# Kernel optimization log

Hardware: AMD Instinct MI355X
Metric: run time of the kernel (lower is better)

Reference implementation:

```python
import jax, jax.numpy as jnp
import numpy as np

N, E, B = 8000, 128000, 16
DIN, D, H, C, L = 16, 256, 8, 32, 6
MC, NT = 200, 8
NEG_SLOPE = 0.2


def layernorm(x, s, b):
    mu = jnp.mean(x, axis=-1, keepdims=True)
    var = jnp.mean(jnp.square(x - mu), axis=-1, keepdims=True)
    return (x - mu) * jax.lax.rsqrt(var + 1e-5) * s + b


def setup_inputs() -> dict:
    key = jax.random.key(0)
    ks = iter(jax.random.split(key, 64))
    rn = lambda shape, s=0.05: jax.random.normal(next(ks), shape, jnp.float32) * s
    inp = {}
    inp['x'] = jax.random.normal(next(ks), (N, DIN), jnp.float32)
    inp['edge_index'] = jax.random.randint(next(ks), (2, E), 0, N)
    inp['batch'] = jnp.sort(jax.random.randint(next(ks), (N,), 0, B))
    # node encoder: Linear(DIN,D) + LayerNorm
    inp['enc_W'] = rn((DIN, D)); inp['enc_b'] = jnp.zeros((D,), jnp.float32)
    inp['enc_ls'] = jnp.ones((D,), jnp.float32); inp['enc_lb'] = jnp.zeros((D,), jnp.float32)
    # GATv2 layers (stacked): lin_l, lin_r, att, output bias, post LayerNorm
    inp['Wl'] = rn((L, D, D)); inp['bl'] = jnp.zeros((L, D), jnp.float32)
    inp['Wr'] = rn((L, D, D)); inp['br'] = jnp.zeros((L, D), jnp.float32)
    inp['att'] = rn((L, H, C))
    inp['gb'] = jnp.zeros((L, D), jnp.float32)
    inp['gls'] = jnp.ones((L, D), jnp.float32); inp['glb'] = jnp.zeros((L, D), jnp.float32)
    # color head MLP: D -> D -> D//2 -> MC
    inp['cW1'] = rn((D, D)); inp['cb1'] = jnp.zeros((D,), jnp.float32)
    inp['cW2'] = rn((D, D // 2)); inp['cb2'] = jnp.zeros((D // 2,), jnp.float32)
    inp['cW3'] = rn((D // 2, MC)); inp['cb3'] = jnp.zeros((MC,), jnp.float32)
    # chromatic head: 2D -> D -> D//2 -> MC
    inp['chW1'] = rn((2 * D, D)); inp['chb1'] = jnp.zeros((D,), jnp.float32)
    inp['chW2'] = rn((D, D // 2)); inp['chb2'] = jnp.zeros((D // 2,), jnp.float32)
    inp['chW3'] = rn((D // 2, MC)); inp['chb3'] = jnp.zeros((MC,), jnp.float32)
    # type head: 2D -> 128 -> NT
    inp['tW1'] = rn((2 * D, 128)); inp['tb1'] = jnp.zeros((128,), jnp.float32)
    inp['tW2'] = rn((128, NT)); inp['tb2'] = jnp.zeros((NT,), jnp.float32)
    # difficulty head: 2D -> 64 -> 1, sigmoid * 100
    inp['dW1'] = rn((2 * D, 64)); inp['db1'] = jnp.zeros((64,), jnp.float32)
    inp['dW2'] = rn((64, 1)); inp['db2'] = jnp.zeros((1,), jnp.float32)
    return inp


def reference(x, edge_index, batch, enc_W, enc_b, enc_ls, enc_lb,
              Wl, bl, Wr, br, att, gb, gls, glb,
              cW1, cb1, cW2, cb2, cW3, cb3,
              chW1, chb1, chW2, chb2, chW3, chb3,
              tW1, tb1, tW2, tb2, dW1, db1, dW2, db2):
    n = x.shape[0]
    # node encoder (dropout = identity at inference)
    h = jax.nn.relu(layernorm(x @ enc_W + enc_b, enc_ls, enc_lb))
    # add self loops once (same for every layer)
    sl = jnp.arange(n)
    src = jnp.concatenate([edge_index[0], sl])  # message source j
    dst = jnp.concatenate([edge_index[1], sl])  # message target i
    for i in range(L):
        xl = (h @ Wl[i] + bl[i]).reshape(n, H, C)  # source transform
        xr = (h @ Wr[i] + br[i]).reshape(n, H, C)  # target transform
        # GATv2 attention: a^T LeakyReLU(xl_j + xr_i)
        e = jax.nn.leaky_relu(xl[src] + xr[dst], NEG_SLOPE)  # [E+N, H, C]
        logits = jnp.einsum('ehc,hc->eh', e, att[i])          # [E+N, H]
        # segment softmax over destination node (self-loops guarantee denom > 0)
        m = jax.ops.segment_max(logits, dst, num_segments=n)
        m = jnp.where(jnp.isfinite(m), m, 0.0)
        p = jnp.exp(logits - m[dst])
        denom = jax.ops.segment_sum(p, dst, num_segments=n)
        alpha = p / denom[dst]
        out = jax.ops.segment_sum(xl[src] * alpha[:, :, None], dst, num_segments=n)
        out = out.reshape(n, D) + gb[i]
        h_new = jax.nn.elu(layernorm(out, gls[i], glb[i]))
        h = h + h_new if i > 0 else h_new
    # per-node color logits
    z = jax.nn.relu(h @ cW1 + cb1)
    z = jax.nn.relu(z @ cW2 + cb2)
    node_colors = z @ cW3 + cb3
    # global mean/max pooling per graph
    cnt = jax.ops.segment_sum(jnp.ones((n,), h.dtype), batch, num_segments=B)
    mean_p = jax.ops.segment_sum(h, batch, num_segments=B) / jnp.maximum(cnt, 1.0)[:, None]
    max_p = jax.ops.segment_max(h, batch, num_segments=B)
    max_p = jnp.where(jnp.isfinite(max_p), max_p, 0.0)
    g = jnp.concatenate([mean_p, max_p], axis=1)  # [B, 2D]
    zc = jax.nn.relu(g @ chW1 + chb1)
    zc = jax.nn.relu(zc @ chW2 + chb2)
    chromatic_num = zc @ chW3 + chb3
    zt = jax.nn.relu(g @ tW1 + tb1)
    graph_type = zt @ tW2 + tb2
    zd = jax.nn.relu(g @ dW1 + db1)
    difficulty = jax.nn.sigmoid(zd @ dW2 + db2) * 100.0
    return (node_colors, chromatic_num, graph_type, difficulty)
```

## Files before the change

### kernel.cpp

```cpp
#include <hip/hip_runtime.h>
#include <hip/hip_bf16.h>

constexpr int DIN = 16;
constexpr int D   = 256;
constexpr int NH  = 8;
constexpr int NC  = 32;
constexpr int MC  = 200;
constexpr int NT  = 8;
constexpr int BG  = 16;
constexpr int NL  = 6;
constexpr int PS  = 16;
constexpr float NEG = 0.2f;

typedef __attribute__((ext_vector_type(8))) short bfrag;
typedef __attribute__((ext_vector_type(4))) float f32x4;

__device__ inline unsigned short f2bf(float f) {
    unsigned int u = __float_as_uint(f);
    u += 0x7FFFu + ((u >> 16) & 1u);
    return (unsigned short)(u >> 16);
}
__device__ inline float bf2f(unsigned short u) {
    return __uint_as_float((unsigned int)u << 16);
}

__device__ inline float dot_ilp(const float* g, const float* __restrict__ W, int K, int ldw, int t) {
    float a0 = 0.f, a1 = 0.f, a2 = 0.f, a3 = 0.f;
    for (int k = 0; k < K; k += 4) {
        a0 = fmaf(g[k + 0], W[(k + 0) * ldw + t], a0);
        a1 = fmaf(g[k + 1], W[(k + 1) * ldw + t], a1);
        a2 = fmaf(g[k + 2], W[(k + 2) * ldw + t], a2);
        a3 = fmaf(g[k + 3], W[(k + 3) * ldw + t], a3);
    }
    return (a0 + a1) + (a2 + a3);
}


__device__ inline void enc_node(const float* x, const float* W, const float* b, const float* ls,
                                const float* lb, float* h, int n, int lane) {
    int c4 = lane * 4;
    float xs[DIN];
#pragma unroll
    for (int k = 0; k < DIN; k += 4) {
        float4 xv = *(const float4*)&x[n * DIN + k];
        xs[k] = xv.x; xs[k + 1] = xv.y; xs[k + 2] = xv.z; xs[k + 3] = xv.w;
    }
    float4 a = *(const float4*)&b[c4];
#pragma unroll
    for (int k = 0; k < DIN; k++) {
        float4 wv = *(const float4*)&W[k * D + c4];
        a.x = fmaf(xs[k], wv.x, a.x);
        a.y = fmaf(xs[k], wv.y, a.y);
        a.z = fmaf(xs[k], wv.z, a.z);
        a.w = fmaf(xs[k], wv.w, a.w);
    }
    float s = a.x + a.y + a.z + a.w;
#pragma unroll
    for (int msk = 1; msk <= 32; msk <<= 1) s += __shfl_xor(s, msk);
    float mu = s * (1.f / D);
    float4 dv = make_float4(a.x - mu, a.y - mu, a.z - mu, a.w - mu);
    float v2 = dv.x * dv.x + dv.y * dv.y + dv.z * dv.z + dv.w * dv.w;
#pragma unroll
    for (int msk = 1; msk <= 32; msk <<= 1) v2 += __shfl_xor(v2, msk);
    float rstd = rsqrtf(v2 * (1.f / D) + 1e-5f);
    float4 lsv = *(const float4*)&ls[c4];
    float4 lbv = *(const float4*)&lb[c4];
    float4 y = make_float4(fmaxf(dv.x * rstd * lsv.x + lbv.x, 0.f),
                           fmaxf(dv.y * rstd * lsv.y + lbv.y, 0.f),
                           fmaxf(dv.z * rstd * lsv.z + lbv.z, 0.f),
                           fmaxf(dv.w * rstd * lsv.w + lbv.w, 0.f));
    *(float4*)&h[(size_t)n * D + c4] = y;
}

__device__ inline float4 attn_compute(const unsigned short* xl, const unsigned short* xr,
                                      const int* row_ptr, const int* col, const float* att,
                                      const float* gb, const float* gls, const float* glb,
                                      const float* h, int layer, int n, int lane) {
    int c4 = lane * 4;
    ushort4 xr4 = *(const ushort4*)&xr[(size_t)n * D + c4];
    float4 xrv = make_float4(bf2f(xr4.x), bf2f(xr4.y), bf2f(xr4.z), bf2f(xr4.w));
    float4 av  = *(const float4*)&att[c4];
    int beg = row_ptr[n], end = row_ptr[n + 1];
    int deg = end - beg;
    int myc = col[beg + min(lane, deg - 1)];
    float l = 0.f;
    float4 acc = make_float4(0.f, 0.f, 0.f, 0.f);
    auto loadx = [&](int i) -> ushort4 {
        if (i < deg) {
            int s = (i < 64) ? __shfl(myc, i) : col[beg + i];
            return *(const ushort4*)&xl[(size_t)s * D + c4];
        }
        return make_ushort4(0, 0, 0, 0);
    };
    auto step = [&](ushort4 x4) {
        float4 xlv = make_float4(bf2f(x4.x), bf2f(x4.y), bf2f(x4.z), bf2f(x4.w));
        float sx = xlv.x + xrv.x; sx = sx > 0.f ? sx : NEG * sx;
        float sy = xlv.y + xrv.y; sy = sy > 0.f ? sy : NEG * sy;
        float sz = xlv.z + xrv.z; sz = sz > 0.f ? sz : NEG * sz;
        float sw = xlv.w + xrv.w; sw = sw > 0.f ? sw : NEG * sw;
        float z = av.x * sx + av.y * sy + av.z * sz + av.w * sw;
        z += __shfl_xor(z, 1); z += __shfl_xor(z, 2); z += __shfl_xor(z, 4);
        float p = __expf(z);
        l += p;
        acc.x = fmaf(p, xlv.x, acc.x);
        acc.y = fmaf(p, xlv.y, acc.y);
        acc.z = fmaf(p, xlv.z, acc.z);
        acc.w = fmaf(p, xlv.w, acc.w);
    };
    ushort4 b0 = loadx(0), b1 = loadx(1), b2 = loadx(2), b3 = loadx(3);
    int e = 0;
    for (; e + 4 <= deg; e += 4) {
        ushort4 n0 = loadx(e + 4), n1 = loadx(e + 5), n2 = loadx(e + 6), n3 = loadx(e + 7);
        step(b0); step(b1); step(b2); step(b3);
        b0 = n0; b1 = n1; b2 = n2; b3 = n3;
    }
    if (e + 0 < deg) step(b0);
    if (e + 1 < deg) step(b1);
    if (e + 2 < deg) step(b2);
    float4 gbv = *(const float4*)&gb[c4];
    float rl = 1.f / l;
    float4 o = make_float4(acc.x * rl + gbv.x, acc.y * rl + gbv.y,
                           acc.z * rl + gbv.z, acc.w * rl + gbv.w);
    float s = o.x + o.y + o.z + o.w;
#pragma unroll
    for (int msk = 1; msk <= 32; msk <<= 1) s += __shfl_xor(s, msk);
    float mu = s * (1.f / D);
    float4 dv = make_float4(o.x - mu, o.y - mu, o.z - mu, o.w - mu);
    float v2 = dv.x * dv.x + dv.y * dv.y + dv.z * dv.z + dv.w * dv.w;
#pragma unroll
    for (int msk = 1; msk <= 32; msk <<= 1) v2 += __shfl_xor(v2, msk);
    float rstd = rsqrtf(v2 * (1.f / D) + 1e-5f);
    float4 glsv = *(const float4*)&gls[c4];
    float4 glbv = *(const float4*)&glb[c4];
    float y0 = dv.x * rstd * glsv.x + glbv.x;
    float y1 = dv.y * rstd * glsv.y + glbv.y;
    float y2 = dv.z * rstd * glsv.z + glbv.z;
    float y3 = dv.w * rstd * glsv.w + glbv.w;
    y0 = y0 > 0.f ? y0 : expm1f(y0);
    y1 = y1 > 0.f ? y1 : expm1f(y1);
    y2 = y2 > 0.f ? y2 : expm1f(y2);
    y3 = y3 > 0.f ? y3 : expm1f(y3);
    float4 prev = make_float4(0.f, 0.f, 0.f, 0.f);
    if (layer > 0) prev = *(const float4*)&h[(size_t)n * D + c4];
    return make_float4(prev.x + y0, prev.y + y1, prev.z + y2, prev.w + y3);
}

__device__ inline void gemm_one_ct(const unsigned short (*As)[264],
                                   const unsigned short* WpL, const unsigned short* WpR,
                                   const float* bl, const float* br,
                                   unsigned short* xl, unsigned short* xr,
                                   int N, int nb, int ctg, int lane) {
    int m = lane & 15, q = lane >> 4;
    float bLv = bl[ctg * 16 + m];
    float bRv = br[ctg * 16 + m];
    f32x4 accL = (f32x4){bLv, bLv, bLv, bLv};
    f32x4 accR = (f32x4){bRv, bRv, bRv, bRv};
#pragma unroll
    for (int ks = 0; ks < 8; ks++) {
        bfrag af = *(const bfrag*)&As[m][ks * 32 + q * 8];
        size_t off = (((size_t)ctg * 8 + ks) * 64 + lane) * 8;
        bfrag bL = *(const bfrag*)&WpL[off];
        bfrag bR = *(const bfrag*)&WpR[off];
        accL = __builtin_amdgcn_mfma_f32_16x16x32_bf16(af, bL, accL, 0, 0, 0);
        accR = __builtin_amdgcn_mfma_f32_16x16x32_bf16(af, bR, accR, 0, 0, 0);
    }
    int colg = ctg * 16 + m;
#pragma unroll
    for (int reg = 0; reg < 4; reg++) {
        int row = nb + q * 4 + reg;
        if (row < N) {
            xl[(size_t)row * D + colg] = f2bf(accL[reg]);
            xr[(size_t)row * D + colg] = f2bf(accR[reg]);
        }
    }
}

__device__ inline void gemm_core(const unsigned short (*As)[264],
                                 const unsigned short* WpL, const unsigned short* WpR,
                                 const float* bl, const float* br,
                                 unsigned short* xl, unsigned short* xr, int N, int nb, int T) {
    int lane = T & 63, w = T >> 6;
#pragma unroll
    for (int ct = 0; ct < 4; ct++)
        gemm_one_ct(As, WpL, WpR, bl, br, xl, xr, N, nb, w * 4 + ct, lane);
}

__device__ inline void repack_attn_one(const float* Wl, const float* Wr, unsigned short* Wp, int tid) {
    int lane = tid & 63;
    int r1 = tid >> 6;
    int ks = r1 & 7;
    int r2 = r1 >> 3;
    int ct = r2 & 15;
    int mi = r2 >> 4;
    int layer = mi >> 1, mat = mi & 1;
    const float* W = (mat == 0 ? Wl : Wr) + (size_t)layer * D * D;
    int n = ct * 16 + (lane & 15);
    int kb = ks * 32 + (lane >> 4) * 8;
    size_t base = (((size_t)(mi * 16 + ct) * 8 + ks) * 64 + lane) * 8;
#pragma unroll
    for (int j = 0; j < 8; j++) Wp[base + j] = f2bf(W[(size_t)(kb + j) * D + n]);
}

__device__ inline void repack_gen_one(const float* W, unsigned short* Wp, int K, int NCOL, int nks, int tid) {
    int lane = tid & 63;
    int r = tid >> 6;
    int ks = r % nks;
    int ct = r / nks;
    int n = ct * 16 + (lane & 15);
    int kb = ks * 32 + (lane >> 4) * 8;
    size_t base = (((size_t)ct * nks + ks) * 64 + lane) * 8;
#pragma unroll
    for (int j = 0; j < 8; j++) {
        int k = kb + j;
        Wp[base + j] = (n < NCOL && k < K) ? f2bf(W[(size_t)k * NCOL + n]) : (unsigned short)0;
    }
}


__global__ __launch_bounds__(256) void fused_init_k(const float* __restrict__ x, const float* __restrict__ encW,
                                                    const float* __restrict__ encb, const float* __restrict__ encls,
                                                    const float* __restrict__ enclb, float* __restrict__ h, int N,
                                                    const int* __restrict__ dst, int* __restrict__ deg, int E,
                                                    const float* __restrict__ Wl, const float* __restrict__ Wr,
                                                    unsigned short* __restrict__ Wp,
                                                    const float* __restrict__ cW1, unsigned short* __restrict__ cW1p,
                                                    const float* __restrict__ cW2, unsigned short* __restrict__ cW2p,
                                                    const float* __restrict__ cW3, unsigned short* __restrict__ cW3p) {
    int gid = blockIdx.x * 256 + threadIdx.x;
    int lane = threadIdx.x & 63;
    int n = blockIdx.x * 4 + (threadIdx.x >> 6);
    if (n < N) enc_node(x, encW, encb, encls, enclb, h, n, lane);
    if (gid < E) atomicAdd(&deg[dst[gid]], 1);
    if (gid < NL * 2 * 16 * 8 * 64) repack_attn_one(Wl, Wr, Wp, gid);
    if (gid < 16 * 8 * 64) repack_gen_one(cW1, cW1p, D, D, 8, gid);
    if (gid < 8 * 8 * 64)  repack_gen_one(cW2, cW2p, D, 128, 8, gid);
    if (gid < 13 * 4 * 64) repack_gen_one(cW3, cW3p, 128, MC, 4, gid);
}

__global__ __launch_bounds__(1024) void scan_k(const int* __restrict__ deg, int* __restrict__ row_ptr,
                                               int* __restrict__ fill, int N) {
    __shared__ int sd[1024];
    int t = threadIdx.x;
    int chunk = (N + 1023) >> 10;
    int lo = t * chunk, hi = min(lo + chunk, N);
    int s = 0;
    for (int i = lo; i < hi; i++) s += deg[i] + 1;
    sd[t] = s;
    __syncthreads();
    for (int off = 1; off < 1024; off <<= 1) {
        int v = (t >= off) ? sd[t - off] : 0;
        __syncthreads();
        sd[t] += v;
        __syncthreads();
    }
    int run = (t > 0) ? sd[t - 1] : 0;
    for (int i = lo; i < hi; i++) {
        row_ptr[i] = run; fill[i] = run;
        run += deg[i] + 1;
    }
    if (t == 1023) row_ptr[N] = sd[1023];
}

__global__ __launch_bounds__(256) void scatter_gemm0_k(const int* __restrict__ src, const int* __restrict__ dst,
                                                       int* __restrict__ fill, int* __restrict__ col, int E, int N,
                                                       const float* __restrict__ h,
                                                       const unsigned short* __restrict__ WpL,
                                                       const unsigned short* __restrict__ WpR,
                                                       const float* __restrict__ bl, const float* __restrict__ br,
                                                       unsigned short* __restrict__ xl, unsigned short* __restrict__ xr) {
    __shared__ unsigned short As[16][264];
    int T = threadIdx.x;
    int tt = blockIdx.x;
    int ntiles = (N + 15) >> 4;
    if (tt < ntiles) {
        int nb = tt * 16;
#pragma unroll
        for (int r = 0; r < 16; r++) {
            int row = nb + r;
            float v = (row < N) ? h[(size_t)row * D + T] : 0.f;
            As[r][T] = f2bf(v);
        }
        __syncthreads();
        gemm_core(As, WpL, WpR, bl, br, xl, xr, N, nb, T);
    }
    for (int e = blockIdx.x * 256 + T; e < E + N; e += gridDim.x * 256) {
        if (e < E) {
            int p = atomicAdd(&fill[dst[e]], 1);
            col[p] = src[e];
        } else {
            int n = e - E;
            int p = atomicAdd(&fill[n], 1);
            col[p] = n;
        }
    }
}

__global__ __launch_bounds__(256) void sortcol_k(const int* __restrict__ row_ptr,
                                                 int* __restrict__ col, int N) {
    int lane = threadIdx.x & 63;
    int n = blockIdx.x * 4 + (threadIdx.x >> 6);
    if (n >= N) return;
    int beg = row_ptr[n], deg = row_ptr[n + 1] - beg;
    if (deg > 64) return;
    int key = (lane < deg) ? col[beg + lane] : 0x7FFFFFFF;
#pragma unroll
    for (int k = 2; k <= 64; k <<= 1) {
#pragma unroll
        for (int j = k >> 1; j > 0; j >>= 1) {
            int other = __shfl_xor(key, j);
            bool up = ((lane & k) == 0);
            bool takeMin = (((lane & j) == 0) == up);
            key = takeMin ? min(key, other) : max(key, other);
        }
    }
    if (lane < deg) col[beg + lane] = key;
}

__global__ __launch_bounds__(256, 4) void attn_k(const unsigned short* __restrict__ xl_in,
                                                 const unsigned short* __restrict__ xr_in,
                                                 const int* __restrict__ row_ptr, const int* __restrict__ col,
                                                 const float* __restrict__ att, const float* __restrict__ gb,
                                                 const float* __restrict__ gls, const float* __restrict__ glb,
                                                 float* __restrict__ h, int layer, int N) {
    int T = threadIdx.x;
    int lane = T & 63, wv = T >> 6;
    int n = blockIdx.x * 4 + wv;
    if (n >= N) return;
    float4 res = attn_compute(xl_in, xr_in, row_ptr, col, att, gb, gls, glb, h, layer, n, lane);
    *(float4*)&h[(size_t)n * D + lane * 4] = res;
}

__global__ __launch_bounds__(256, 4) void gemm_lr_k(const float* __restrict__ h,
                                                    const unsigned short* __restrict__ WpL,
                                                    const unsigned short* __restrict__ WpR,
                                                    const float* __restrict__ bl, const float* __restrict__ br,
                                                    unsigned short* __restrict__ xl, unsigned short* __restrict__ xr,
                                                    int N) {
    __shared__ unsigned short As[16][264];
    int T = threadIdx.x;
    int nb = blockIdx.x * 16;
#pragma unroll
    for (int r = 0; r < 16; r++) {
        int row = nb + r;
        float v = (row < N) ? h[(size_t)row * D + T] : 0.f;
        As[r][T] = f2bf(v);
    }
    __syncthreads();
    gemm_core(As, WpL, WpR, bl, br, xl, xr, N, nb, T);
}

__global__ __launch_bounds__(1024) void colorhead_k(const float* __restrict__ h, int N,
                                                    const unsigned short* __restrict__ W1p, const float* __restrict__ b1,
                                                    const unsigned short* __restrict__ W2p, const float* __restrict__ b2,
                                                    const unsigned short* __restrict__ W3p, const float* __restrict__ b3,
                                                    float* __restrict__ out) {
    __shared__ unsigned short As[16][264];
    __shared__ unsigned short Zs[16][264];
    int T = threadIdx.x;
    int lane = T & 63, wv = T >> 6;
    int nb = blockIdx.x * 16;
    int c4 = lane * 4;
    int n = nb + wv;
    if (n < N) {
        float4 v = *(const float4*)&h[(size_t)n * D + c4];
        As[wv][c4 + 0] = f2bf(v.x);
        As[wv][c4 + 1] = f2bf(v.y);
        As[wv][c4 + 2] = f2bf(v.z);
        As[wv][c4 + 3] = f2bf(v.w);
    } else {
        As[wv][c4 + 0] = 0; As[wv][c4 + 1] = 0; As[wv][c4 + 2] = 0; As[wv][c4 + 3] = 0;
    }
    __syncthreads();
    int m = lane & 15, q = lane >> 4;
    {
        float bv = b1[wv * 16 + m];
        f32x4 acc = (f32x4){bv, bv, bv, bv};
#pragma unroll
        for (int ks = 0; ks < 8; ks++) {
            bfrag af = *(const bfrag*)&As[m][ks * 32 + q * 8];
            bfrag bf = *(const bfrag*)&W1p[(((size_t)wv * 8 + ks) * 64 + lane) * 8];
            acc = __builtin_amdgcn_mfma_f32_16x16x32_bf16(af, bf, acc, 0, 0, 0);
        }
        int colg = wv * 16 + m;
#pragma unroll
        for (int reg = 0; reg < 4; reg++)
            Zs[q * 4 + reg][colg] = f2bf(fmaxf(acc[reg], 0.f));
    }
    __syncthreads();
    if (wv < 8) {
        float bv = b2[wv * 16 + m];
        f32x4 acc = (f32x4){bv, bv, bv, bv};
#pragma unroll
        for (int ks = 0; ks < 8; ks++) {
            bfrag af = *(const bfrag*)&Zs[m][ks * 32 + q * 8];
            bfrag bf = *(const bfrag*)&W2p[(((size_t)wv * 8 + ks) * 64 + lane) * 8];
            acc = __builtin_amdgcn_mfma_f32_16x16x32_bf16(af, bf, acc, 0, 0, 0);
        }
        int colg = wv * 16 + m;
#pragma unroll
        for (int reg = 0; reg < 4; reg++)
            As[q * 4 + reg][colg] = f2bf(fmaxf(acc[reg], 0.f));
    }
    __syncthreads();
    if (wv < 13) {
        int colg = wv * 16 + m;
        float bv = (colg < MC) ? b3[colg] : 0.f;
        f32x4 acc = (f32x4){bv, bv, bv, bv};
#pragma unroll
        for (int ks = 0; ks < 4; ks++) {
            bfrag af = *(const bfrag*)&As[m][ks * 32 + q * 8];
            bfrag bf = *(const bfrag*)&W3p[(((size_t)wv * 4 + ks) * 64 + lane) * 8];
            acc = __builtin_amdgcn_mfma_f32_16x16x32_bf16(af, bf, acc, 0, 0, 0);
        }
#pragma unroll
        for (int reg = 0; reg < 4; reg++) {
            int row = nb + q * 4 + reg;
            if (row < N && colg < MC) out[(size_t)row * MC + colg] = acc[reg];
        }
    }
}

__global__ __launch_bounds__(256) void pool_k(const float* __restrict__ h, const int* __restrict__ batch,
                                              float* __restrict__ psum, float* __restrict__ pmax,
                                              int* __restrict__ cnt, int N) {
    int b = blockIdx.x;
    int sl = blockIdx.y;
    int c = threadIdx.x;
    int lo = 0, hi = N;
    while (lo < hi) { int mid = (lo + hi) >> 1; if (batch[mid] < b) lo = mid + 1; else hi = mid; }
    int s0 = lo;
    lo = 0; hi = N;
    while (lo < hi) { int mid = (lo + hi) >> 1; if (batch[mid] < b + 1) lo = mid + 1; else hi = mid; }
    int s1 = lo;
    int len = s1 - s0;
    int chunk = (len + PS - 1) / PS;
    int n0 = s0 + sl * chunk;
    int n1 = min(n0 + chunk, s1);
    float sum = 0.f, mx = -3.0e38f;
    for (int n = n0; n < n1; n++) {
        float v = h[(size_t)n * D + c];
        sum += v;
        mx = fmaxf(mx, v);
    }
    psum[(size_t)(b * PS + sl) * D + c] = sum;
    pmax[(size_t)(b * PS + sl) * D + c] = mx;
    if (c == 0 && sl == 0) cnt[b] = len;
}

__global__ __launch_bounds__(256) void heads_k(const float* __restrict__ psum, const float* __restrict__ pmax,
                                               const int* __restrict__ cnt,
                                               const float* __restrict__ chW1, const float* __restrict__ chb1,
                                               const float* __restrict__ chW2, const float* __restrict__ chb2,
                                               const float* __restrict__ chW3, const float* __restrict__ chb3,
                                               const float* __restrict__ tW1, const float* __restrict__ tb1,
                                               const float* __restrict__ tW2, const float* __restrict__ tb2,
                                               const float* __restrict__ dW1, const float* __restrict__ db1,
                                               const float* __restrict__ dW2, const float* __restrict__ db2,
                                               float* __restrict__ out_ch, float* __restrict__ out_t,
                                               float* __restrict__ out_d) {
    int b = blockIdx.x, sec = blockIdx.y, t = threadIdx.x;
    __shared__ float g[2 * D];
    __shared__ float z1[D];
    __shared__ float z2[128];
    float sum = 0.f, mx = -3.0e38f;
#pragma unroll
    for (int sl = 0; sl < PS; sl++) {
        sum += psum[(size_t)(b * PS + sl) * D + t];
        mx = fmaxf(mx, pmax[(size_t)(b * PS + sl) * D + t]);
    }
    int cn = cnt[b];
    float c = fmaxf((float)cn, 1.f);
    g[t] = sum / c;
    g[D + t] = (cn > 0) ? mx : 0.f;
    __syncthreads();
    if (sec == 0) {
        z1[t] = fmaxf(chb1[t] + dot_ilp(g, chW1, 2 * D, D, t), 0.f);
        __syncthreads();
        if (t < 128) z2[t] = fmaxf(chb2[t] + dot_ilp(z1, chW2, D, 128, t), 0.f);
        __syncthreads();
        if (t < MC) out_ch[b * MC + t] = chb3[t] + dot_ilp(z2, chW3, 128, MC, t);
    } else if (sec == 1) {
        if (t < 128) z1[t] = fmaxf(tb1[t] + dot_ilp(g, tW1, 2 * D, 128, t), 0.f);
        __syncthreads();
        if (t < NT) out_t[b * NT + t] = tb2[t] + dot_ilp(z1, tW2, 128, NT, t);
    } else {
        if (t < 64) z1[t] = fmaxf(db1[t] + dot_ilp(g, dW1, 2 * D, 64, t), 0.f);
        __syncthreads();
        if (t == 0) {
            float a = db2[0] + dot_ilp(z1, dW2, 64, 1, 0);
            out_d[b] = 100.f / (1.f + __expf(-a));
        }
    }
}

extern "C" void kernel_launch(void* const* d_in, const int* in_sizes, int n_in,
                              void* d_out, int out_size, void* d_ws, size_t ws_size,
                              hipStream_t stream) {
    const float* x     = (const float*)d_in[0];
    const int*   ei    = (const int*)d_in[1];
    const int*   batch = (const int*)d_in[2];
    const float* encW  = (const float*)d_in[3];
    const float* encb  = (const float*)d_in[4];
    const float* encls = (const float*)d_in[5];
    const float* enclb = (const float*)d_in[6];
    const float* Wl    = (const float*)d_in[7];
    const float* bl    = (const float*)d_in[8];
    const float* Wr    = (const float*)d_in[9];
    const float* br    = (const float*)d_in[10];
    const float* att   = (const float*)d_in[11];
    const float* gb    = (const float*)d_in[12];
    const float* gls   = (const float*)d_in[13];
    const float* glb   = (const float*)d_in[14];
    const float* cW1   = (const float*)d_in[15];
    const float* cb1   = (const float*)d_in[16];
    const float* cW2   = (const float*)d_in[17];
    const float* cb2   = (const float*)d_in[18];
    const float* cW3   = (const float*)d_in[19];
    const float* cb3   = (const float*)d_in[20];
    const float* chW1  = (const float*)d_in[21];
    const float* chb1  = (const float*)d_in[22];
    const float* chW2  = (const float*)d_in[23];
    const float* chb2  = (const float*)d_in[24];
    const float* chW3  = (const float*)d_in[25];
    const float* chb3  = (const float*)d_in[26];
    const float* tW1   = (const float*)d_in[27];
    const float* tb1   = (const float*)d_in[28];
    const float* tW2   = (const float*)d_in[29];
    const float* tb2   = (const float*)d_in[30];
    const float* dW1   = (const float*)d_in[31];
    const float* db1   = (const float*)d_in[32];
    const float* dW2   = (const float*)d_in[33];
    const float* db2   = (const float*)d_in[34];

    const int N = in_sizes[0] / DIN;
    const int E = in_sizes[1] / 2;
    const int* esrc = ei;
    const int* edst = ei + E;

    char* p = (char*)d_ws;
    auto carve = [&](size_t bytes) { char* r = p; p += (bytes + 255) & ~(size_t)255; return r; };
    int*            row_ptr = (int*)carve((size_t)(N + 1) * 4);
    int*            fill    = (int*)carve((size_t)N * 4);
    int*            deg     = (int*)carve((size_t)N * 4);
    int*            cnt     = (int*)carve((size_t)BG * 4);
    float*          psum    = (float*)carve((size_t)BG * PS * D * 4);
    float*          pmax    = (float*)carve((size_t)BG * PS * D * 4);
    int*            col     = (int*)carve((size_t)(E + N) * 4);
    unsigned short* Wp      = (unsigned short*)carve((size_t)NL * 2 * 65536 * 2);
    unsigned short* cW1p    = (unsigned short*)carve((size_t)16 * 8 * 64 * 8 * 2);
    unsigned short* cW2p    = (unsigned short*)carve((size_t)8 * 8 * 64 * 8 * 2);
    unsigned short* cW3p    = (unsigned short*)carve((size_t)13 * 4 * 64 * 8 * 2);
    float*          h       = (float*)carve((size_t)N * D * 4);
    unsigned short* xlA     = (unsigned short*)carve((size_t)N * D * 2);
    unsigned short* xrA     = (unsigned short*)carve((size_t)N * D * 2);
    unsigned short* xlB     = (unsigned short*)carve((size_t)N * D * 2);
    unsigned short* xrB     = (unsigned short*)carve((size_t)N * D * 2);
    (void)ws_size; (void)n_in; (void)out_size;

    const int ntiles16 = (N + 15) / 16;
    const int nblk4    = (N + 3) / 4;
    const int sblocks  = max(ntiles16, (E + N + 255) / 256);
    const int fblocks  = max((N + 3) / 4, max((E + 255) / 256, 384));

    hipMemsetAsync(deg, 0, (size_t)N * 4, stream);
    fused_init_k<<<fblocks, 256, 0, stream>>>(x, encW, encb, encls, enclb, h, N,
                                              edst, deg, E, Wl, Wr, Wp,
                                              cW1, cW1p, cW2, cW2p, cW3, cW3p);
    scan_k<<<1, 1024, 0, stream>>>(deg, row_ptr, fill, N);
    scatter_gemm0_k<<<sblocks, 256, 0, stream>>>(esrc, edst, fill, col, E, N, h,
                                                 Wp + 0, Wp + (size_t)65536,
                                                 bl + 0, br + 0, xlA, xrA);
    sortcol_k<<<nblk4, 256, 0, stream>>>(row_ptr, col, N);
    for (int l = 0; l < NL - 1; l++) {
        const unsigned short* xin_l = (l & 1) ? xlB : xlA;
        const unsigned short* xin_r = (l & 1) ? xrB : xrA;
        unsigned short* xout_l = (l & 1) ? xlA : xlB;
        unsigned short* xout_r = (l & 1) ? xrA : xrB;
        attn_k<<<nblk4, 256, 0, stream>>>(xin_l, xin_r, row_ptr, col, att + l * NH * NC,
                                          gb + l * D, gls + l * D, glb + l * D, h, l, N);
        gemm_lr_k<<<ntiles16, 256, 0, stream>>>(h,
                                                Wp + (size_t)((l + 1) * 2 + 0) * 65536,
                                                Wp + (size_t)((l + 1) * 2 + 1) * 65536,
                                                bl + (l + 1) * D, br + (l + 1) * D, xout_l, xout_r, N);
    }
    float* out = (float*)d_out;
    attn_k<<<nblk4, 256, 0, stream>>>(xlB, xrB, row_ptr, col, att + (NL - 1) * NH * NC,
                                      gb + (NL - 1) * D, gls + (NL - 1) * D, glb + (NL - 1) * D,
                                      h, NL - 1, N);
    colorhead_k<<<ntiles16, 1024, 0, stream>>>(h, N, cW1p, cb1, cW2p, cb2, cW3p, cb3, out);
    pool_k<<<dim3(BG, PS), 256, 0, stream>>>(h, batch, psum, pmax, cnt, N);
    heads_k<<<dim3(BG, 3), 256, 0, stream>>>(psum, pmax, cnt, chW1, chb1, chW2, chb2, chW3, chb3,
                                             tW1, tb1, tW2, tb2, dW1, db1, dW2, db2,
                                             out + (size_t)N * MC,
                                             out + (size_t)N * MC + BG * MC,
                                             out + (size_t)N * MC + BG * MC + BG * NT);
}
```

Measured before the change: 417.8 us.

## Split wavefront across two edges per step and fold column sort into first attention

```diff
diff --git a/kernel.cpp b/kernel.cpp
--- a/kernel.cpp
+++ b/kernel.cpp
@@ -70,79 +70,6 @@
                            fmaxf(dv.z * rstd * lsv.z + lbv.z, 0.f),
                            fmaxf(dv.w * rstd * lsv.w + lbv.w, 0.f));
     *(float4*)&h[(size_t)n * D + c4] = y;
-}
-
-__device__ inline float4 attn_compute(const unsigned short* xl, const unsigned short* xr,
-                                      const int* row_ptr, const int* col, const float* att,
-                                      const float* gb, const float* gls, const float* glb,
-                                      const float* h, int layer, int n, int lane) {
-    int c4 = lane * 4;
-    ushort4 xr4 = *(const ushort4*)&xr[(size_t)n * D + c4];
-    float4 xrv = make_float4(bf2f(xr4.x), bf2f(xr4.y), bf2f(xr4.z), bf2f(xr4.w));
-    float4 av  = *(const float4*)&att[c4];
-    int beg = row_ptr[n], end = row_ptr[n + 1];
-    int deg = end - beg;
-    int myc = col[beg + min(lane, deg - 1)];
-    float l = 0.f;
-    float4 acc = make_float4(0.f, 0.f, 0.f, 0.f);
-    auto loadx = [&](int i) -> ushort4 {
-        if (i < deg) {
-            int s = (i < 64) ? __shfl(myc, i) : col[beg + i];
-            return *(const ushort4*)&xl[(size_t)s * D + c4];
-        }
-        return make_ushort4(0, 0, 0, 0);
-    };
-    auto step = [&](ushort4 x4) {
-        float4 xlv = make_float4(bf2f(x4.x), bf2f(x4.y), bf2f(x4.z), bf2f(x4.w));
-        float sx = xlv.x + xrv.x; sx = sx > 0.f ? sx : NEG * sx;
-        float sy = xlv.y + xrv.y; sy = sy > 0.f ? sy : NEG * sy;
-        float sz = xlv.z + xrv.z; sz = sz > 0.f ? sz : NEG * sz;
-        float sw = xlv.w + xrv.w; sw = sw > 0.f ? sw : NEG * sw;
-        float z = av.x * sx + av.y * sy + av.z * sz + av.w * sw;
-        z += __shfl_xor(z, 1); z += __shfl_xor(z, 2); z += __shfl_xor(z, 4);
-        float p = __expf(z);
-        l += p;
-        acc.x = fmaf(p, xlv.x, acc.x);
-        acc.y = fmaf(p, xlv.y, acc.y);
-        acc.z = fmaf(p, xlv.z, acc.z);
-        acc.w = fmaf(p, xlv.w, acc.w);
-    };
-    ushort4 b0 = loadx(0), b1 = loadx(1), b2 = loadx(2), b3 = loadx(3);
-    int e = 0;
-    for (; e + 4 <= deg; e += 4) {
-        ushort4 n0 = loadx(e + 4), n1 = loadx(e + 5), n2 = loadx(e + 6), n3 = loadx(e + 7);
-        step(b0); step(b1); step(b2); step(b3);
-        b0 = n0; b1 = n1; b2 = n2; b3 = n3;
-    }
-    if (e + 0 < deg) step(b0);
-    if (e + 1 < deg) step(b1);
-    if (e + 2 < deg) step(b2);
-    float4 gbv = *(const float4*)&gb[c4];
-    float rl = 1.f / l;
-    float4 o = make_float4(acc.x * rl + gbv.x, acc.y * rl + gbv.y,
-                           acc.z * rl + gbv.z, acc.w * rl + gbv.w);
-    float s = o.x + o.y + o.z + o.w;
-#pragma unroll
-    for (int msk = 1; msk <= 32; msk <<= 1) s += __shfl_xor(s, msk);
-    float mu = s * (1.f / D);
-    float4 dv = make_float4(o.x - mu, o.y - mu, o.z - mu, o.w - mu);
-    float v2 = dv.x * dv.x + dv.y * dv.y + dv.z * dv.z + dv.w * dv.w;
-#pragma unroll
-    for (int msk = 1; msk <= 32; msk <<= 1) v2 += __shfl_xor(v2, msk);
-    float rstd = rsqrtf(v2 * (1.f / D) + 1e-5f);
-    float4 glsv = *(const float4*)&gls[c4];
-    float4 glbv = *(const float4*)&glb[c4];
-    float y0 = dv.x * rstd * glsv.x + glbv.x;
-    float y1 = dv.y * rstd * glsv.y + glbv.y;
-    float y2 = dv.z * rstd * glsv.z + glbv.z;
-    float y3 = dv.w * rstd * glsv.w + glbv.w;
-    y0 = y0 > 0.f ? y0 : expm1f(y0);
-    y1 = y1 > 0.f ? y1 : expm1f(y1);
-    y2 = y2 > 0.f ? y2 : expm1f(y2);
-    y3 = y3 > 0.f ? y3 : expm1f(y3);
-    float4 prev = make_float4(0.f, 0.f, 0.f, 0.f);
-    if (layer > 0) prev = *(const float4*)&h[(size_t)n * D + c4];
-    return make_float4(prev.x + y0, prev.y + y1, prev.z + y2, prev.w + y3);
 }
 
 __device__ inline void gemm_one_ct(const unsigned short (*As)[264],
@@ -295,30 +222,9 @@
     }
 }
 
-__global__ __launch_bounds__(256) void sortcol_k(const int* __restrict__ row_ptr,
-                                                 int* __restrict__ col, int N) {
-    int lane = threadIdx.x & 63;
-    int n = blockIdx.x * 4 + (threadIdx.x >> 6);
-    if (n >= N) return;
-    int beg = row_ptr[n], deg = row_ptr[n + 1] - beg;
-    if (deg > 64) return;
-    int key = (lane < deg) ? col[beg + lane] : 0x7FFFFFFF;
-#pragma unroll
-    for (int k = 2; k <= 64; k <<= 1) {
-#pragma unroll
-        for (int j = k >> 1; j > 0; j >>= 1) {
-            int other = __shfl_xor(key, j);
-            bool up = ((lane & k) == 0);
-            bool takeMin = (((lane & j) == 0) == up);
-            key = takeMin ? min(key, other) : max(key, other);
-        }
-    }
-    if (lane < deg) col[beg + lane] = key;
-}
-
 __global__ __launch_bounds__(256, 4) void attn_k(const unsigned short* __restrict__ xl_in,
                                                  const unsigned short* __restrict__ xr_in,
-                                                 const int* __restrict__ row_ptr, const int* __restrict__ col,
+                                                 const int* __restrict__ row_ptr, int* __restrict__ col,
                                                  const float* __restrict__ att, const float* __restrict__ gb,
                                                  const float* __restrict__ gls, const float* __restrict__ glb,
                                                  float* __restrict__ h, int layer, int N) {
@@ -326,8 +232,122 @@
     int lane = T & 63, wv = T >> 6;
     int n = blockIdx.x * 4 + wv;
     if (n >= N) return;
-    float4 res = attn_compute(xl_in, xr_in, row_ptr, col, att, gb, gls, glb, h, layer, n, lane);
-    *(float4*)&h[(size_t)n * D + lane * 4] = res;
+    int half = lane >> 5, sub = lane & 31, c8 = sub * 8;
+    int beg = row_ptr[n], deg = row_ptr[n + 1] - beg;
+    int myc = col[beg + min(lane, deg - 1)];
+    if (layer == 0 && deg <= 64) {
+        int key = (lane < deg) ? myc : 0x7FFFFFFF;
+#pragma unroll
+        for (int k = 2; k <= 64; k <<= 1) {
+#pragma unroll
+            for (int j = k >> 1; j > 0; j >>= 1) {
+                int other = __shfl_xor(key, j);
+                bool up = ((lane & k) == 0);
+                key = ((((lane & j) == 0) == up) ? min(key, other) : max(key, other));
+            }
+        }
+        if (lane < deg) col[beg + lane] = key;
+        myc = key;
+    }
+    float xrv[8], av[8], acc[8] = {0.f, 0.f, 0.f, 0.f, 0.f, 0.f, 0.f, 0.f};
+    {
+        const unsigned short* xp = &xr_in[(size_t)n * D + c8];
+        ushort4 r0 = *(const ushort4*)xp;
+        ushort4 r1 = *(const ushort4*)(xp + 4);
+        xrv[0] = bf2f(r0.x); xrv[1] = bf2f(r0.y); xrv[2] = bf2f(r0.z); xrv[3] = bf2f(r0.w);
+        xrv[4] = bf2f(r1.x); xrv[5] = bf2f(r1.y); xrv[6] = bf2f(r1.z); xrv[7] = bf2f(r1.w);
+        float4 a0 = *(const float4*)&att[c8];
+        float4 a1 = *(const float4*)&att[c8 + 4];
+        av[0] = a0.x; av[1] = a0.y; av[2] = a0.z; av[3] = a0.w;
+        av[4] = a1.x; av[5] = a1.y; av[6] = a1.z; av[7] = a1.w;
+    }
+    float l = 0.f;
+    auto loadp = [&](int i) -> bfrag {
+        int eidx = 2 * i + half;
+        if (eidx < deg) {
+            int s = (eidx < 64) ? __shfl(myc, eidx) : col[beg + eidx];
+            return *(const bfrag*)&xl_in[(size_t)s * D + c8];
+        }
+        bfrag z = {0, 0, 0, 0, 0, 0, 0, 0};
+        return z;
+    };
+    auto step = [&](bfrag x8, int i) {
+        float xlv[8];
+#pragma unroll
+        for (int j = 0; j < 8; j++) xlv[j] = bf2f((unsigned short)x8[j]);
+        float z = 0.f;
+#pragma unroll
+        for (int j = 0; j < 8; j++) {
+            float s = xlv[j] + xrv[j];
+            s = s > 0.f ? s : NEG * s;
+            z = fmaf(av[j], s, z);
+        }
+        z += __shfl_xor(z, 1);
+        z += __shfl_xor(z, 2);
+        float p = __expf(z);
+        p = (2 * i + half < deg) ? p : 0.f;
+        l += p;
+#pragma unroll
+        for (int j = 0; j < 8; j++) acc[j] = fmaf(p, xlv[j], acc[j]);
+    };
+    int S = (deg + 1) >> 1;
+    bfrag b0 = loadp(0), b1 = loadp(1), b2 = loadp(2), b3 = loadp(3);
+    int i = 0;
+    for (; i + 4 <= S; i += 4) {
+        bfrag q0 = loadp(i + 4), q1 = loadp(i + 5), q2 = loadp(i + 6), q3 = loadp(i + 7);
+        step(b0, i); step(b1, i + 1); step(b2, i + 2); step(b3, i + 3);
+        b0 = q0; b1 = q1; b2 = q2; b3 = q3;
+    }
+    if (i     < S) step(b0, i);
+    if (i + 1 < S) step(b1, i + 1);
+    if (i + 2 < S) step(b2, i + 2);
+    l += __shfl_xor(l, 32);
+#pragma unroll
+    for (int j = 0; j < 8; j++) acc[j] += __shfl_xor(acc[j], 32);
+    float rl = 1.f / l;
+    float o[8];
+    {
+        float4 g0 = *(const float4*)&gb[c8];
+        float4 g1 = *(const float4*)&gb[c8 + 4];
+        float gv[8] = {g0.x, g0.y, g0.z, g0.w, g1.x, g1.y, g1.z, g1.w};
+#pragma unroll
+        for (int j = 0; j < 8; j++) o[j] = acc[j] * rl + gv[j];
+    }
+    float s = 0.f;
+#pragma unroll
+    for (int j = 0; j < 8; j++) s += o[j];
+#pragma unroll
+    for (int msk = 1; msk <= 16; msk <<= 1) s += __shfl_xor(s, msk);
+    float mu = s * (1.f / D);
+    float dv[8];
+    float v2 = 0.f;
+#pragma unroll
+    for (int j = 0; j < 8; j++) { dv[j] = o[j] - mu; v2 = fmaf(dv[j], dv[j], v2); }
+#pragma unroll
+    for (int msk = 1; msk <= 16; msk <<= 1) v2 += __shfl_xor(v2, msk);
+    float rstd = rsqrtf(v2 * (1.f / D) + 1e-5f);
+    if (half == 0) {
+        float4 s0 = *(const float4*)&gls[c8];
+        float4 s1 = *(const float4*)&gls[c8 + 4];
+        float4 t0 = *(const float4*)&glb[c8];
+        float4 t1 = *(const float4*)&glb[c8 + 4];
+        float sv[8] = {s0.x, s0.y, s0.z, s0.w, s1.x, s1.y, s1.z, s1.w};
+        float tv[8] = {t0.x, t0.y, t0.z, t0.w, t1.x, t1.y, t1.z, t1.w};
+        float out[8];
+#pragma unroll
+        for (int j = 0; j < 8; j++) {
+            float y = dv[j] * rstd * sv[j] + tv[j];
+            out[j] = y > 0.f ? y : expm1f(y);
+        }
+        if (layer > 0) {
+            float4 p0 = *(const float4*)&h[(size_t)n * D + c8];
+            float4 p1 = *(const float4*)&h[(size_t)n * D + c8 + 4];
+            out[0] += p0.x; out[1] += p0.y; out[2] += p0.z; out[3] += p0.w;
+            out[4] += p1.x; out[5] += p1.y; out[6] += p1.z; out[7] += p1.w;
+        }
+        *(float4*)&h[(size_t)n * D + c8]     = make_float4(out[0], out[1], out[2], out[3]);
+        *(float4*)&h[(size_t)n * D + c8 + 4] = make_float4(out[4], out[5], out[6], out[7]);
+    }
 }
 
 __global__ __launch_bounds__(256, 4) void gemm_lr_k(const float* __restrict__ h,
@@ -570,7 +590,6 @@
     scatter_gemm0_k<<<sblocks, 256, 0, stream>>>(esrc, edst, fill, col, E, N, h,
                                                  Wp + 0, Wp + (size_t)65536,
                                                  bl + 0, br + 0, xlA, xrA);
-    sortcol_k<<<nblk4, 256, 0, stream>>>(row_ptr, col, N);
     for (int l = 0; l < NL - 1; l++) {
         const unsigned short* xin_l = (l & 1) ? xlB : xlA;
         const unsigned short* xin_r = (l & 1) ? xrB : xrA;
```

New measurement: 422.0 us. No clear change (+1.0%).

## Keep a bf16 copy of node state for GEMM staging and deepen edge prefetch

Applied to the files above, without the earlier changes.

```diff
diff --git a/kernel.cpp b/kernel.cpp
--- a/kernel.cpp
+++ b/kernel.cpp
@@ -37,7 +37,7 @@
 
 
 __device__ inline void enc_node(const float* x, const float* W, const float* b, const float* ls,
-                                const float* lb, float* h, int n, int lane) {
+                                const float* lb, float* h, unsigned short* hb, int n, int lane) {
     int c4 = lane * 4;
     float xs[DIN];
 #pragma unroll
@@ -70,6 +70,8 @@
                            fmaxf(dv.z * rstd * lsv.z + lbv.z, 0.f),
                            fmaxf(dv.w * rstd * lsv.w + lbv.w, 0.f));
     *(float4*)&h[(size_t)n * D + c4] = y;
+    ushort4 yb = make_ushort4(f2bf(y.x), f2bf(y.y), f2bf(y.z), f2bf(y.w));
+    *(ushort4*)&hb[(size_t)n * D + c4] = yb;
 }
 
 __device__ inline float4 attn_compute(const unsigned short* xl, const unsigned short* xr,
@@ -108,15 +110,25 @@
         acc.w = fmaf(p, xlv.w, acc.w);
     };
     ushort4 b0 = loadx(0), b1 = loadx(1), b2 = loadx(2), b3 = loadx(3);
+    ushort4 b4 = loadx(4), b5 = loadx(5), b6 = loadx(6), b7 = loadx(7);
     int e = 0;
-    for (; e + 4 <= deg; e += 4) {
-        ushort4 n0 = loadx(e + 4), n1 = loadx(e + 5), n2 = loadx(e + 6), n3 = loadx(e + 7);
-        step(b0); step(b1); step(b2); step(b3);
-        b0 = n0; b1 = n1; b2 = n2; b3 = n3;
+    for (; e + 8 <= deg; e += 8) {
+        step(b0); b0 = loadx(e + 8);
+        step(b1); b1 = loadx(e + 9);
+        step(b2); b2 = loadx(e + 10);
+        step(b3); b3 = loadx(e + 11);
+        step(b4); b4 = loadx(e + 12);
+        step(b5); b5 = loadx(e + 13);
+        step(b6); b6 = loadx(e + 14);
+        step(b7); b7 = loadx(e + 15);
     }
     if (e + 0 < deg) step(b0);
     if (e + 1 < deg) step(b1);
     if (e + 2 < deg) step(b2);
+    if (e + 3 < deg) step(b3);
+    if (e + 4 < deg) step(b4);
+    if (e + 5 < deg) step(b5);
+    if (e + 6 < deg) step(b6);
     float4 gbv = *(const float4*)&gb[c4];
     float rl = 1.f / l;
     float4 o = make_float4(acc.x * rl + gbv.x, acc.y * rl + gbv.y,
@@ -185,6 +197,17 @@
         gemm_one_ct(As, WpL, WpR, bl, br, xl, xr, N, nb, w * 4 + ct, lane);
 }
 
+__device__ inline void stage_hb(const unsigned short* hb, unsigned short (*As)[264],
+                                int nb, int N, int T) {
+    for (int i = T; i < 16 * 128; i += 256) {
+        int r = i >> 7, c = i & 127;
+        int row = nb + r;
+        unsigned int v = 0;
+        if (row < N) v = *(const unsigned int*)&hb[(size_t)row * D + 2 * c];
+        *(unsigned int*)&As[r][2 * c] = v;
+    }
+}
+
 __device__ inline void repack_attn_one(const float* Wl, const float* Wr, unsigned short* Wp, int tid) {
     int lane = tid & 63;
     int r1 = tid >> 6;
@@ -219,7 +242,8 @@
 
 __global__ __launch_bounds__(256) void fused_init_k(const float* __restrict__ x, const float* __restrict__ encW,
                                                     const float* __restrict__ encb, const float* __restrict__ encls,
-                                                    const float* __restrict__ enclb, float* __restrict__ h, int N,
+                                                    const float* __restrict__ enclb, float* __restrict__ h,
+                                                    unsigned short* __restrict__ hb, int N,
                                                     const int* __restrict__ dst, int* __restrict__ deg, int E,
                                                     const float* __restrict__ Wl, const float* __restrict__ Wr,
                                                     unsigned short* __restrict__ Wp,
@@ -229,7 +253,7 @@
     int gid = blockIdx.x * 256 + threadIdx.x;
     int lane = threadIdx.x & 63;
     int n = blockIdx.x * 4 + (threadIdx.x >> 6);
-    if (n < N) enc_node(x, encW, encb, encls, enclb, h, n, lane);
+    if (n < N) enc_node(x, encW, encb, encls, enclb, h, hb, n, lane);
     if (gid < E) atomicAdd(&deg[dst[gid]], 1);
     if (gid < NL * 2 * 16 * 8 * 64) repack_attn_one(Wl, Wr, Wp, gid);
     if (gid < 16 * 8 * 64) repack_gen_one(cW1, cW1p, D, D, 8, gid);
@@ -263,7 +287,7 @@
 
 __global__ __launch_bounds__(256) void scatter_gemm0_k(const int* __restrict__ src, const int* __restrict__ dst,
                                                        int* __restrict__ fill, int* __restrict__ col, int E, int N,
-                                                       const float* __restrict__ h,
+                                                       const unsigned short* __restrict__ hb,
                                                        const unsigned short* __restrict__ WpL,
                                                        const unsigned short* __restrict__ WpR,
                                                        const float* __restrict__ bl, const float* __restrict__ br,
@@ -273,15 +297,9 @@
     int tt = blockIdx.x;
     int ntiles = (N + 15) >> 4;
     if (tt < ntiles) {
-        int nb = tt * 16;
-#pragma unroll
-        for (int r = 0; r < 16; r++) {
-            int row = nb + r;
-            float v = (row < N) ? h[(size_t)row * D + T] : 0.f;
-            As[r][T] = f2bf(v);
-        }
+        stage_hb(hb, As, tt * 16, N, T);
         __syncthreads();
-        gemm_core(As, WpL, WpR, bl, br, xl, xr, N, nb, T);
+        gemm_core(As, WpL, WpR, bl, br, xl, xr, N, tt * 16, T);
     }
     for (int e = blockIdx.x * 256 + T; e < E + N; e += gridDim.x * 256) {
         if (e < E) {
@@ -321,16 +339,20 @@
                                                  const int* __restrict__ row_ptr, const int* __restrict__ col,
                                                  const float* __restrict__ att, const float* __restrict__ gb,
                                                  const float* __restrict__ gls, const float* __restrict__ glb,
-                                                 float* __restrict__ h, int layer, int N) {
+                                                 float* __restrict__ h, unsigned short* __restrict__ hb,
+                                                 int layer, int N) {
     int T = threadIdx.x;
     int lane = T & 63, wv = T >> 6;
     int n = blockIdx.x * 4 + wv;
     if (n >= N) return;
     float4 res = attn_compute(xl_in, xr_in, row_ptr, col, att, gb, gls, glb, h, layer, n, lane);
-    *(float4*)&h[(size_t)n * D + lane * 4] = res;
-}
-
-__global__ __launch_bounds__(256, 4) void gemm_lr_k(const float* __restrict__ h,
+    int c4 = lane * 4;
+    *(float4*)&h[(size_t)n * D + c4] = res;
+    ushort4 rb = make_ushort4(f2bf(res.x), f2bf(res.y), f2bf(res.z), f2bf(res.w));
+    *(ushort4*)&hb[(size_t)n * D + c4] = rb;
+}
+
+__global__ __launch_bounds__(256, 4) void gemm_lr_k(const unsigned short* __restrict__ hb,
                                                     const unsigned short* __restrict__ WpL,
                                                     const unsigned short* __restrict__ WpR,
                                                     const float* __restrict__ bl, const float* __restrict__ br,
@@ -339,17 +361,12 @@
     __shared__ unsigned short As[16][264];
     int T = threadIdx.x;
     int nb = blockIdx.x * 16;
-#pragma unroll
-    for (int r = 0; r < 16; r++) {
-        int row = nb + r;
-        float v = (row < N) ? h[(size_t)row * D + T] : 0.f;
-        As[r][T] = f2bf(v);
-    }
+    stage_hb(hb, As, nb, N, T);
     __syncthreads();
     gemm_core(As, WpL, WpR, bl, br, xl, xr, N, nb, T);
 }
 
-__global__ __launch_bounds__(1024) void colorhead_k(const float* __restrict__ h, int N,
+__global__ __launch_bounds__(1024) void colorhead_k(const unsigned short* __restrict__ hb, int N,
                                                     const unsigned short* __restrict__ W1p, const float* __restrict__ b1,
                                                     const unsigned short* __restrict__ W2p, const float* __restrict__ b2,
                                                     const unsigned short* __restrict__ W3p, const float* __restrict__ b3,
@@ -362,11 +379,7 @@
     int c4 = lane * 4;
     int n = nb + wv;
     if (n < N) {
-        float4 v = *(const float4*)&h[(size_t)n * D + c4];
-        As[wv][c4 + 0] = f2bf(v.x);
-        As[wv][c4 + 1] = f2bf(v.y);
-        As[wv][c4 + 2] = f2bf(v.z);
-        As[wv][c4 + 3] = f2bf(v.w);
+        *(ushort4*)&As[wv][c4] = *(const ushort4*)&hb[(size_t)n * D + c4];
     } else {
         As[wv][c4 + 0] = 0; As[wv][c4 + 1] = 0; As[wv][c4 + 2] = 0; As[wv][c4 + 3] = 0;
     }
@@ -551,6 +564,7 @@
     unsigned short* cW2p    = (unsigned short*)carve((size_t)8 * 8 * 64 * 8 * 2);
     unsigned short* cW3p    = (unsigned short*)carve((size_t)13 * 4 * 64 * 8 * 2);
     float*          h       = (float*)carve((size_t)N * D * 4);
+    unsigned short* hb      = (unsigned short*)carve((size_t)N * D * 2);
     unsigned short* xlA     = (unsigned short*)carve((size_t)N * D * 2);
     unsigned short* xrA     = (unsigned short*)carve((size_t)N * D * 2);
     unsigned short* xlB     = (unsigned short*)carve((size_t)N * D * 2);
@@ -563,11 +577,11 @@
     const int fblocks  = max((N + 3) / 4, max((E + 255) / 256, 384));
 
     hipMemsetAsync(deg, 0, (size_t)N * 4, stream);
-    fused_init_k<<<fblocks, 256, 0, stream>>>(x, encW, encb, encls, enclb, h, N,
+    fused_init_k<<<fblocks, 256, 0, stream>>>(x, encW, encb, encls, enclb, h, hb, N,
                                               edst, deg, E, Wl, Wr, Wp,
                                               cW1, cW1p, cW2, cW2p, cW3, cW3p);
     scan_k<<<1, 1024, 0, stream>>>(deg, row_ptr, fill, N);
-    scatter_gemm0_k<<<sblocks, 256, 0, stream>>>(esrc, edst, fill, col, E, N, h,
+    scatter_gemm0_k<<<sblocks, 256, 0, stream>>>(esrc, edst, fill, col, E, N, hb,
                                                  Wp + 0, Wp + (size_t)65536,
                                                  bl + 0, br + 0, xlA, xrA);
     sortcol_k<<<nblk4, 256, 0, stream>>>(row_ptr, col, N);
@@ -577,8 +591,8 @@
         unsigned short* xout_l = (l & 1) ? xlA : xlB;
         unsigned short* xout_r = (l & 1) ? xrA : xrB;
         attn_k<<<nblk4, 256, 0, stream>>>(xin_l, xin_r, row_ptr, col, att + l * NH * NC,
-                                          gb + l * D, gls + l * D, glb + l * D, h, l, N);
-        gemm_lr_k<<<ntiles16, 256, 0, stream>>>(h,
+                                          gb + l * D, gls + l * D, glb + l * D, h, hb, l, N);
+        gemm_lr_k<<<ntiles16, 256, 0, stream>>>(hb,
                                                 Wp + (size_t)((l + 1) * 2 + 0) * 65536,
                                                 Wp + (size_t)((l + 1) * 2 + 1) * 65536,
                                                 bl + (l + 1) * D, br + (l + 1) * D, xout_l, xout_r, N);
@@ -586,8 +600,8 @@
     float* out = (float*)d_out;
     attn_k<<<nblk4, 256, 0, stream>>>(xlB, xrB, row_ptr, col, att + (NL - 1) * NH * NC,
                                       gb + (NL - 1) * D, gls + (NL - 1) * D, glb + (NL - 1) * D,
-                                      h, NL - 1, N);
-    colorhead_k<<<ntiles16, 1024, 0, stream>>>(h, N, cW1p, cb1, cW2p, cb2, cW3p, cb3, out);
+                                      h, hb, NL - 1, N);
+    colorhead_k<<<ntiles16, 1024, 0, stream>>>(hb, N, cW1p, cb1, cW2p, cb2, cW3p, cb3, out);
     pool_k<<<dim3(BG, PS), 256, 0, stream>>>(h, batch, psum, pmax, cnt, N);
     heads_k<<<dim3(BG, 3), 256, 0, stream>>>(psum, pmax, cnt, chW1, chb1, chW2, chb2, chW3, chb3,
                                              tW1, tb1, tW2, tb2, dW1, db1, dW2, db2,
```

Result: slower. 429.5 us (+2.8%).
